# Performance work log

Measured on AMD Instinct MI355X. Metric: run time of the kernel, lower is better.

## Reference

```python
import jax, jax.numpy as jnp
import numpy as np
from jax import lax

POOL_OUT = 20  # SOCA AdaptiveAvgPool2d((20,20))
MID = 16       # out_channel // 2
BN_EPS = 1e-3


def _pool_matrix(n, out):
    # Row-stochastic matrix replicating torch AdaptiveAvgPool2d bin boundaries:
    # start = floor(i*n/out), end = ceil((i+1)*n/out)
    P = np.zeros((out, n), np.float32)
    for i in range(out):
        s = (i * n) // out
        e = -((-(i + 1) * n) // out)
        P[i, s:e] = 1.0 / (e - s)
    return jnp.asarray(P)


def setup_inputs() -> dict:
    key = jax.random.key(0)
    ks = jax.random.split(key, 5)
    B, C, H, W = 16, 256, 128, 128
    OC = 32
    x = jax.random.normal(ks[0], (B, C, H, W), dtype=jnp.float32)
    linear_w = jax.random.normal(ks[1], (C, C), dtype=jnp.float32) * (1.0 / np.sqrt(C))
    linear_b = jnp.zeros((C,), jnp.float32)
    lsa_w = jax.random.normal(ks[2], (1, 2, 7, 7), dtype=jnp.float32) * 0.1  # Conv2d(2,1,7) no bias
    conv_w = jax.random.normal(ks[3], (OC, OC, 3, 3), dtype=jnp.float32) * (1.0 / np.sqrt(OC * 9))
    conv_b = jnp.zeros((OC,), jnp.float32)
    bn_gamma = jnp.ones((OC,), jnp.float32)
    bn_beta = jnp.zeros((OC,), jnp.float32)
    return {"x": x, "linear_w": linear_w, "linear_b": linear_b, "lsa_w": lsa_w,
            "conv_w": conv_w, "conv_b": conv_b, "bn_gamma": bn_gamma, "bn_beta": bn_beta}


def _bsa_forward(x, linear_w, linear_b, lsa_w, conv_w, conv_b, bn_gamma, bn_beta):
    b, c, h, w = x.shape
    # ---- SOCA: second-order channel attention ----
    PH = _pool_matrix(h, POOL_OUT)
    PW = _pool_matrix(w, POOL_OUT)
    xp = jnp.einsum('oh,bchw,pw->bcop', PH, x, PW)          # (b,c,20,20)
    n = POOL_OUT * POOL_OUT
    v = xp.reshape(b, c, n).transpose(0, 2, 1)               # (b,400,c)
    vc = v - v.mean(axis=1, keepdims=True)
    cov = jnp.einsum('bnc,bnd->bcd', vc, vc) / (n - 1)       # (b,c,c)
    feat = cov.mean(axis=2)                                  # (b,c)
    attn = jax.nn.sigmoid(feat @ linear_w.T + linear_b)      # (b,c)
    # ---- channel scoring / top-k selection ----
    score = attn.mean(axis=0)                                # (c,)
    score_id = jnp.argsort(-score)                           # descending
    max_id = jnp.sort(score_id[:MID])                        # (MID,)
    x1 = jnp.take(x, max_id, axis=1) * (1.0 + score[max_id])[None, :, None, None]
    # ---- grouped channel mean (c divisible by MID by construction) ----
    g = c // MID
    x2 = x.reshape(b, MID, g, h, w).mean(axis=2)             # (b,MID,h,w)
    xc = jnp.concatenate([x1, x2], axis=1)                   # (b,32,h,w)
    # ---- LSA spatial attention ----
    s = jnp.concatenate([xc.mean(axis=1, keepdims=True),
                         xc.max(axis=1, keepdims=True)], axis=1)  # (b,2,h,w)
    a = lax.conv_general_dilated(s, lsa_w, (1, 1), [(3, 3), (3, 3)],
                                 dimension_numbers=('NCHW', 'OIHW', 'NCHW'))
    xa = xc * jax.nn.sigmoid(a)
    # ---- CBA: conv(3x3, stride 2) + BN(train stats) + SiLU ----
    y = lax.conv_general_dilated(xa, conv_w, (2, 2), [(1, 1), (1, 1)],
                                 dimension_numbers=('NCHW', 'OIHW', 'NCHW'))
    y = y + conv_b[None, :, None, None]
    mu = y.mean(axis=(0, 2, 3))
    var = y.var(axis=(0, 2, 3))
    yn = (y - mu[None, :, None, None]) * lax.rsqrt(var + BN_EPS)[None, :, None, None]
    yn = yn * bn_gamma[None, :, None, None] + bn_beta[None, :, None, None]
    return yn * jax.nn.sigmoid(yn)  # SiLU


def reference(x, linear_w, linear_b, lsa_w, conv_w, conv_b, bn_gamma, bn_beta):
    return _bsa_forward(x, linear_w, linear_b, lsa_w, conv_w, conv_b, bn_gamma, bn_beta)
```

## Files before the change

### kernel.cpp

```cpp
#include <hip/hip_runtime.h>
#include <math.h>

#define B_ 16
#define C_ 256
#define H_ 128
#define W_ 128
#define HW_ (H_*W_)
#define PO 20
#define NPOOL (PO*PO)
#define MID_ 16
#define OC_ 32
#define OH_ 64
#define OW_ 64
#define BN_EPS 1e-3f

#define OFF_XP     0
#define OFF_SN     1638400
#define OFF_SCORE  1648896
#define OFF_BNSUM  1649184
#define OFF_BNSQ   1649216
#define OFF_SMEAN  1649248
#define OFF_SMAX   1911392
#define OFF_SIGA   2173536
#define OFF_XC     2435680

__device__ __forceinline__ int bin_s(int p) { return (p * 128) / 20; }
__device__ __forceinline__ int bin_e(int p) { return ((p + 1) * 128 + 19) / 20; }

__global__ __launch_bounds__(256) void k_pool2(const float* __restrict__ x,
                                               float* __restrict__ xp,
                                               float* __restrict__ sn,
                                               float* __restrict__ xc) {
  __shared__ float tmp[2][64 * 21];
  const int blk = blockIdx.x;
  const int b = blk >> 5, g = (blk >> 1) & 15, rh = blk & 1;
  const int tid = threadIdx.x;
  const int hl = tid >> 2, q = tid & 3;
  const int hg = rh * 64 + hl;
  const float* rowbase = x + (size_t)(b * C_) * HW_ + (size_t)hg * W_ + q * 32;

  float4 xacc[8];
#pragma unroll
  for (int j = 0; j < 8; ++j) xacc[j] = make_float4(0.f, 0.f, 0.f, 0.f);
  float snacc = 0.f;

  float4 cur[8], nxt[8];
  {
    const float4* s4 = (const float4*)(rowbase + (size_t)(g * 16) * HW_);
#pragma unroll
    for (int j = 0; j < 8; ++j) cur[j] = s4[j];
  }

#pragma unroll
  for (int k = 0; k < 16; ++k) {
    if (k < 15) {
      const float4* s4 = (const float4*)(rowbase + (size_t)(g * 16 + k + 1) * HW_);
#pragma unroll
      for (int j = 0; j < 8; ++j) nxt[j] = s4[j];
    }
    const int c = g * 16 + k;
    float bin[5];
#pragma unroll
    for (int p = 0; p < 5; ++p) bin[p] = 0.f;
#pragma unroll
    for (int j = 0; j < 8; ++j) {
      float4 v = cur[j];
      xacc[j].x += v.x; xacc[j].y += v.y; xacc[j].z += v.z; xacc[j].w += v.w;
      const float c4[4] = {v.x, v.y, v.z, v.w};
#pragma unroll
      for (int kk = 0; kk < 4; ++kk) {
        const int cc = 4 * j + kk;
#pragma unroll
        for (int p = 0; p < 5; ++p) {
          const int S = (p * 32) / 5;
          const int E = ((p + 1) * 32 + 4) / 5;
          if (cc >= S && cc < E) bin[p] += c4[kk];
        }
      }
    }
    float* tb = tmp[k & 1];
#pragma unroll
    for (int p = 0; p < 5; ++p) {
      const int S = (p * 32) / 5, E = ((p + 1) * 32 + 4) / 5;
      tb[hl * 21 + q * 5 + p] = bin[p] / (float)(E - S);
    }
    asm volatile("s_waitcnt lgkmcnt(0)\n\ts_barrier" ::: "memory");
    if (tid < 200) {
      const int ol = tid / 20, p = tid % 20;
      const int o = rh * 10 + ol;
      const int rs_ = bin_s(o), re_ = bin_e(o);
      float s = 0.f;
      for (int r = rs_; r < re_; ++r) s += tb[(r - rh * 64) * 21 + p];
      float v = s / (float)(re_ - rs_);
      xp[(size_t)(b * C_ + c) * NPOOL + o * PO + p] = v;
      snacc += v;
    }
    if (k < 15) {
#pragma unroll
      for (int j = 0; j < 8; ++j) cur[j] = nxt[j];
    }
  }
  if (tid < 200) atomicAdd(&sn[b * NPOOL + rh * 200 + tid], snacc);
  float4* dst = (float4*)(xc + (size_t)(b * OC_ + MID_ + g) * HW_ + (size_t)hg * W_ + q * 32);
#pragma unroll
  for (int j = 0; j < 8; ++j) {
    float4 v = xacc[j];
    v.x *= 0.0625f; v.y *= 0.0625f; v.z *= 0.0625f; v.w *= 0.0625f;
    dst[j] = v;
  }
}

__global__ __launch_bounds__(256) void k_featattn(const float* __restrict__ xp,
                                                  const float* __restrict__ sn,
                                                  const float* __restrict__ lw,
                                                  const float* __restrict__ lb,
                                                  float* __restrict__ score) {
  const int b = blockIdx.x;
  const int tid = threadIdx.x;
  __shared__ float snl[NPOOL];
  __shared__ float red[256];
  __shared__ float featl[C_];
  for (int i = tid; i < NPOOL; i += 256) snl[i] = sn[b * NPOOL + i];
  __syncthreads();
  const float4* row4 = (const float4*)(xp + (size_t)(b * C_ + tid) * NPOOL);
  float rs = 0.f, dot = 0.f;
#pragma unroll 4
  for (int n = 0; n < NPOOL / 4; ++n) {
    float4 v = row4[n];
    rs += v.x + v.y + v.z + v.w;
    dot += v.x * snl[4 * n] + v.y * snl[4 * n + 1]
         + v.z * snl[4 * n + 2] + v.w * snl[4 * n + 3];
  }
  red[tid] = rs;
  __syncthreads();
  for (int s = 128; s > 0; s >>= 1) {
    if (tid < s) red[tid] += red[tid + s];
    __syncthreads();
  }
  const float totm = red[0] / (float)NPOOL;
  featl[tid] = (dot - totm * rs) / ((float)(NPOOL - 1) * (float)C_);
  __syncthreads();
  const float4* wrow = (const float4*)(lw + (size_t)tid * C_);
  float z = 0.f;
#pragma unroll 4
  for (int i = 0; i < C_ / 4; ++i) {
    float4 w = wrow[i];
    z += w.x * featl[4 * i] + w.y * featl[4 * i + 1]
       + w.z * featl[4 * i + 2] + w.w * featl[4 * i + 3];
  }
  z += lb[tid];
  float sig = 1.0f / (1.0f + expf(-z));
  atomicAdd(&score[tid], sig * (1.0f / (float)B_));
}

__global__ __launch_bounds__(256) void k_build(const float* __restrict__ x,
                                               const float* __restrict__ score,
                                               float* __restrict__ xc,
                                               float* __restrict__ smean,
                                               float* __restrict__ smax) {
  __shared__ float ss[C_];
  __shared__ int flag[C_];
  __shared__ int mid_s[MID_];
  __shared__ float sc_s[MID_];
  __shared__ float4 ps[128], pm[128];
  const int tid = threadIdx.x;
  ss[tid] = score[tid];
  __syncthreads();
  {
    float my = ss[tid];
    int rank = 0;
    for (int k = 0; k < C_; ++k) {
      float v = ss[k];
      rank += (v > my || (v == my && k < tid)) ? 1 : 0;
    }
    flag[tid] = (rank < MID_) ? 1 : 0;
    __syncthreads();
    if (rank < MID_) {
      int pos = 0;
      for (int k = 0; k < tid; ++k) pos += flag[k];
      mid_s[pos] = tid;
      sc_s[pos] = 1.0f + my;
    }
  }
  __syncthreads();
  const int p = tid & 127, s = tid >> 7;
  const int P = blockIdx.x * 128 + p;
  const int b = P >> 12, pix4 = P & 4095;
  const float4* xb = (const float4*)x + (size_t)(b * C_) * (HW_ / 4) + pix4;
  float4* xcb = (float4*)xc + (size_t)(b * OC_) * (HW_ / 4) + pix4;
  float4 ms = make_float4(0.f, 0.f, 0.f, 0.f);
  float4 mx = make_float4(-INFINITY, -INFINITY, -INFINITY, -INFINITY);
#pragma unroll
  for (int mi = 0; mi < 8; ++mi) {
    int m = s * 8 + mi;
    float4 t = xb[(size_t)mid_s[m] * (HW_ / 4)];
    float sc = sc_s[m];
    t.x *= sc; t.y *= sc; t.z *= sc; t.w *= sc;
    xcb[(size_t)m * (HW_ / 4)] = t;
    ms.x += t.x; ms.y += t.y; ms.z += t.z; ms.w += t.w;
    mx.x = fmaxf(mx.x, t.x); mx.y = fmaxf(mx.y, t.y);
    mx.z = fmaxf(mx.z, t.z); mx.w = fmaxf(mx.w, t.w);
  }
#pragma unroll
  for (int gi = 0; gi < 8; ++gi) {
    float4 t = xcb[(size_t)(MID_ + s * 8 + gi) * (HW_ / 4)];
    ms.x += t.x; ms.y += t.y; ms.z += t.z; ms.w += t.w;
    mx.x = fmaxf(mx.x, t.x); mx.y = fmaxf(mx.y, t.y);
    mx.z = fmaxf(mx.z, t.z); mx.w = fmaxf(mx.w, t.w);
  }
  if (s == 1) { ps[p] = ms; pm[p] = mx; }
  __syncthreads();
  if (s == 0) {
    float4 a = ps[p], m2 = pm[p];
    ms.x = (ms.x + a.x) * (1.f / 32.f); ms.y = (ms.y + a.y) * (1.f / 32.f);
    ms.z = (ms.z + a.z) * (1.f / 32.f); ms.w = (ms.w + a.w) * (1.f / 32.f);
    mx.x = fmaxf(mx.x, m2.x); mx.y = fmaxf(mx.y, m2.y);
    mx.z = fmaxf(mx.z, m2.z); mx.w = fmaxf(mx.w, m2.w);
    ((float4*)smean)[P] = ms;
    ((float4*)smax)[P] = mx;
  }
}

__global__ __launch_bounds__(256) void k_lsa(const float* __restrict__ smean,
                                             const float* __restrict__ smax,
                                             const float* __restrict__ lsa_w,
                                             float* __restrict__ siga) {
  __shared__ float w0[49], w1[49];
  if (threadIdx.x < 49) {
    w0[threadIdx.x] = lsa_w[threadIdx.x];
    w1[threadIdx.x] = lsa_w[49 + threadIdx.x];
  }
  __syncthreads();
  int idx = blockIdx.x * 256 + threadIdx.x;
  int b = idx >> 14;
  int pix = idx & (HW_ - 1);
  int h = pix >> 7, w = pix & 127;
  const float* pm = smean + (size_t)b * HW_;
  const float* px = smax + (size_t)b * HW_;
  float acc = 0.f;
  for (int kh = 0; kh < 7; ++kh) {
    int ih = h + kh - 3;
    if (ih < 0 || ih >= H_) continue;
    for (int kw = 0; kw < 7; ++kw) {
      int iw = w + kw - 3;
      if (iw < 0 || iw >= W_) continue;
      int p = ih * W_ + iw;
      acc += pm[p] * w0[kh * 7 + kw] + px[p] * w1[kh * 7 + kw];
    }
  }
  siga[idx] = 1.0f / (1.0f + __expf(-acc));
}

__global__ __launch_bounds__(256) void k_conv(const float* __restrict__ xc,
                                              const float* __restrict__ siga,
                                              const float* __restrict__ conv_w,
                                              const float* __restrict__ conv_b,
                                              float* __restrict__ out,
                                              float* __restrict__ bnsum,
                                              float* __restrict__ bnsq) {
  __shared__ __attribute__((aligned(16))) float in_lds[4 * 5 * 132];
  __shared__ float sg_lds[5 * 132];
  __shared__ float w_lds[288 * 33];
  const int tid = threadIdx.x;
  const int oc = tid & 31;
  const int g = tid >> 5;
  const int b = blockIdx.x >> 5;
  const int oh0 = (blockIdx.x & 31) * 2;
  const int ih0 = 2 * oh0 - 1;

  for (int i = tid; i < 288 * 32; i += 256) {
    int oc_ = i / 288, rem = i % 288;
    w_lds[rem * 33 + oc_] = conv_w[i];
  }
  const float* sgb = siga + (size_t)b * HW_;
  for (int i = tid; i < 5 * 132; i += 256) {
    int r = i / 132, col = i % 132;
    int ih = ih0 + r, iw = col - 1;
    float v = 0.f;
    if (ih >= 0 && ih < H_ && iw >= 0 && iw < W_) v = sgb[ih * W_ + iw];
    sg_lds[i] = v;
  }

  float acc[2][8];
#pragma unroll
  for (int a = 0; a < 2; ++a)
#pragma unroll
    for (int o = 0; o < 8; ++o) acc[a][o] = 0.f;

  for (int chunk = 0; chunk < 8; ++chunk) {
    __syncthreads();
    for (int i = tid; i < 4 * 5 * 132; i += 256) {
      int icl = i / 660;
      int rem = i % 660;
      int r = rem / 132, col = rem % 132;
      int ih = ih0 + r, iw = col - 1;
      float v = 0.f;
      if (ih >= 0 && ih < H_ && iw >= 0 && iw < W_) {
        v = xc[((size_t)(b * OC_) + (chunk * 4 + icl)) * HW_ + ih * W_ + iw] * sg_lds[rem];
      }
      in_lds[i] = v;
    }
    __syncthreads();
#pragma unroll
    for (int icl = 0; icl < 4; ++icl) {
      float wr[9];
      const int wb = (chunk * 4 + icl) * 9 * 33 + oc;
#pragma unroll
      for (int t = 0; t < 9; ++t) wr[t] = w_lds[wb + t * 33];
#pragma unroll
      for (int r = 0; r < 5; ++r) {
        float f[20] __attribute__((aligned(16)));
        const float4* s4 = (const float4*)&in_lds[(icl * 5 + r) * 132 + 16 * g];
#pragma unroll
        for (int j = 0; j < 5; ++j) ((float4*)f)[j] = s4[j];
#pragma unroll
        for (int ohl = 0; ohl < 2; ++ohl) {
          const int kh = r - 2 * ohl;
          if (kh < 0 || kh > 2) continue;
          float w0 = wr[kh * 3 + 0];
          float w1 = wr[kh * 3 + 1];
          float w2 = wr[kh * 3 + 2];
#pragma unroll
          for (int o = 0; o < 8; ++o)
            acc[ohl][o] += f[2 * o] * w0 + f[2 * o + 1] * w1 + f[2 * o + 2] * w2;
        }
      }
    }
  }

  float bias = conv_b[oc];
  float lsum = 0.f, lsq = 0.f;
  float* outp = out + ((size_t)(b * OC_) + oc) * (OH_ * OW_) + (size_t)oh0 * OW_ + g * 8;
#pragma unroll
  for (int ohl = 0; ohl < 2; ++ohl) {
    float vout[8] __attribute__((aligned(16)));
#pragma unroll
    for (int o = 0; o < 8; ++o) {
      float v = acc[ohl][o] + bias;
      vout[o] = v;
      lsum += v;
      lsq += v * v;
    }
    *((float4*)(outp + ohl * OW_)) = *(float4*)&vout[0];
    *((float4*)(outp + ohl * OW_ + 4)) = *(float4*)&vout[4];
  }
  __syncthreads();
  in_lds[tid] = lsum;
  in_lds[256 + tid] = lsq;
  __syncthreads();
  if (tid < 32) {
    float t = 0.f, tq = 0.f;
#pragma unroll
    for (int gg = 0; gg < 8; ++gg) {
      t += in_lds[gg * 32 + tid];
      tq += in_lds[256 + gg * 32 + tid];
    }
    atomicAdd(&bnsum[tid], t);
    atomicAdd(&bnsq[tid], tq);
  }
}

__global__ __launch_bounds__(256) void k_apply(float* __restrict__ out,
                                               const float* __restrict__ sum,
                                               const float* __restrict__ sq,
                                               const float* __restrict__ gamma,
                                               const float* __restrict__ beta) {
  __shared__ float ssc[OC_], ssh[OC_];
  if (threadIdx.x < OC_) {
    int i = threadIdx.x;
    const float N = (float)(B_ * OH_ * OW_);
    float mu = sum[i] / N;
    float var = sq[i] / N - mu * mu;
    float sc = gamma[i] / sqrtf(var + BN_EPS);
    ssc[i] = sc;
    ssh[i] = beta[i] - mu * sc;
  }
  __syncthreads();
  int idx4 = blockIdx.x * 256 + threadIdx.x;
  int oc = (idx4 >> 10) & 31;
  float sc = ssc[oc], sh = ssh[oc];
  float4 v = ((float4*)out)[idx4];
  float t;
  t = v.x * sc + sh; v.x = t / (1.0f + __expf(-t));
  t = v.y * sc + sh; v.y = t / (1.0f + __expf(-t));
  t = v.z * sc + sh; v.z = t / (1.0f + __expf(-t));
  t = v.w * sc + sh; v.w = t / (1.0f + __expf(-t));
  ((float4*)out)[idx4] = v;
}

extern "C" void kernel_launch(void* const* d_in, const int* in_sizes, int n_in,
                              void* d_out, int out_size, void* d_ws, size_t ws_size,
                              hipStream_t stream) {
  const float* x      = (const float*)d_in[0];
  const float* lw     = (const float*)d_in[1];
  const float* lb     = (const float*)d_in[2];
  const float* lsa_w  = (const float*)d_in[3];
  const float* conv_w = (const float*)d_in[4];
  const float* conv_b = (const float*)d_in[5];
  const float* gamma  = (const float*)d_in[6];
  const float* beta   = (const float*)d_in[7];
  float* out = (float*)d_out;
  float* ws = (float*)d_ws;

  hipMemsetAsync(ws + OFF_SN, 0,
                 (size_t)(OFF_BNSQ + OC_ - OFF_SN) * sizeof(float), stream);

  k_pool2<<<512, 256, 0, stream>>>(x, ws + OFF_XP, ws + OFF_SN, ws + OFF_XC);
  k_featattn<<<B_, 256, 0, stream>>>(ws + OFF_XP, ws + OFF_SN, lw, lb, ws + OFF_SCORE);
  k_build<<<512, 256, 0, stream>>>(x, ws + OFF_SCORE, ws + OFF_XC,
                                   ws + OFF_SMEAN, ws + OFF_SMAX);
  k_lsa<<<1024, 256, 0, stream>>>(ws + OFF_SMEAN, ws + OFF_SMAX, lsa_w, ws + OFF_SIGA);
  k_conv<<<512, 256, 0, stream>>>(ws + OFF_XC, ws + OFF_SIGA, conv_w, conv_b, out,
                                  ws + OFF_BNSUM, ws + OFF_BNSQ);
  k_apply<<<2048, 256, 0, stream>>>(out, ws + OFF_BNSUM, ws + OFF_BNSQ, gamma, beta);
}
```

Before: 504.2 us.

## Fuse all stages into one persistent kernel with software grid barriers

Replaces the six separate kernel launches with a single 512-block kernel. The stages are separated by atomic-counter grid barriers in workspace memory. The feature/attention step is also spread over all 512 blocks instead of 16, using warp-level reductions and an extra per-batch totm atomic. The goal is to remove launch gaps and the serialised low-parallelism featattn kernel. In exchange it drops the register double-buffering prefetch in the pool stage and relies on all 512 blocks being co-resident for the spin barriers to work. The barrier has a guard timeout that could silently break ordering.

New measurement: 898.8 us. +78.3%, slower.

```diff
diff --git a/kernel.cpp b/kernel.cpp
--- a/kernel.cpp
+++ b/kernel.cpp
@@ -16,376 +16,407 @@
 
 #define OFF_XP     0
 #define OFF_SN     1638400
+#define OFF_BAR    1644800
 #define OFF_SCORE  1648896
+#define OFF_TOTM   1649152
 #define OFF_BNSUM  1649184
 #define OFF_BNSQ   1649216
 #define OFF_SMEAN  1649248
 #define OFF_SMAX   1911392
 #define OFF_SIGA   2173536
 #define OFF_XC     2435680
+#define OFF_RS     10824288
+#define OFF_DOT    10828384
 
 __device__ __forceinline__ int bin_s(int p) { return (p * 128) / 20; }
 __device__ __forceinline__ int bin_e(int p) { return ((p + 1) * 128 + 19) / 20; }
 
-__global__ __launch_bounds__(256) void k_pool2(const float* __restrict__ x,
-                                               float* __restrict__ xp,
-                                               float* __restrict__ sn,
-                                               float* __restrict__ xc) {
-  __shared__ float tmp[2][64 * 21];
+__device__ __forceinline__ void gbar(unsigned* bar, unsigned target) {
+  __syncthreads();
+  if (threadIdx.x == 0) {
+    __threadfence();
+    __hip_atomic_fetch_add(bar, 1u, __ATOMIC_RELEASE, __HIP_MEMORY_SCOPE_AGENT);
+    long guard = 0;
+    while (__hip_atomic_load(bar, __ATOMIC_ACQUIRE, __HIP_MEMORY_SCOPE_AGENT) < target) {
+      __builtin_amdgcn_s_sleep(8);
+      if (++guard > (1L << 22)) break;
+    }
+  }
+  __syncthreads();
+}
+
+__global__ __launch_bounds__(256, 2) void mega(
+    const float* __restrict__ x, const float* __restrict__ lw,
+    const float* __restrict__ lb, const float* __restrict__ lsa_w,
+    const float* __restrict__ conv_w, const float* __restrict__ conv_b,
+    const float* __restrict__ gamma, const float* __restrict__ beta,
+    float* __restrict__ out, float* __restrict__ ws) {
+  __shared__ __attribute__((aligned(16))) float smem[13000];
   const int blk = blockIdx.x;
-  const int b = blk >> 5, g = (blk >> 1) & 15, rh = blk & 1;
   const int tid = threadIdx.x;
-  const int hl = tid >> 2, q = tid & 3;
-  const int hg = rh * 64 + hl;
-  const float* rowbase = x + (size_t)(b * C_) * HW_ + (size_t)hg * W_ + q * 32;
-
-  float4 xacc[8];
-#pragma unroll
-  for (int j = 0; j < 8; ++j) xacc[j] = make_float4(0.f, 0.f, 0.f, 0.f);
-  float snacc = 0.f;
-
-  float4 cur[8], nxt[8];
-  {
-    const float4* s4 = (const float4*)(rowbase + (size_t)(g * 16) * HW_);
-#pragma unroll
-    for (int j = 0; j < 8; ++j) cur[j] = s4[j];
-  }
-
-#pragma unroll
-  for (int k = 0; k < 16; ++k) {
-    if (k < 15) {
-      const float4* s4 = (const float4*)(rowbase + (size_t)(g * 16 + k + 1) * HW_);
-#pragma unroll
-      for (int j = 0; j < 8; ++j) nxt[j] = s4[j];
-    }
-    const int c = g * 16 + k;
-    float bin[5];
-#pragma unroll
-    for (int p = 0; p < 5; ++p) bin[p] = 0.f;
+  float* xp    = ws + OFF_XP;
+  float* sn    = ws + OFF_SN;
+  unsigned* bar = (unsigned*)(ws + OFF_BAR);
+  float* score = ws + OFF_SCORE;
+  float* totm  = ws + OFF_TOTM;
+  float* bnsum = ws + OFF_BNSUM;
+  float* bnsq  = ws + OFF_BNSQ;
+  float* smean = ws + OFF_SMEAN;
+  float* smax  = ws + OFF_SMAX;
+  float* siga  = ws + OFF_SIGA;
+  float* xc    = ws + OFF_XC;
+  float* rsb   = ws + OFF_RS;
+  float* dotb  = ws + OFF_DOT;
+
+  {
+    float (*tmp)[64 * 21] = (float (*)[64 * 21])smem;
+    const int b = blk >> 5, g = (blk >> 1) & 15, rh = blk & 1;
+    const int hl = tid >> 2, q = tid & 3;
+    const int hg = rh * 64 + hl;
+    const float* rowbase = x + (size_t)(b * C_) * HW_ + (size_t)hg * W_ + q * 32;
+
+    float4 xacc[8];
+#pragma unroll
+    for (int j = 0; j < 8; ++j) xacc[j] = make_float4(0.f, 0.f, 0.f, 0.f);
+    float snacc = 0.f;
+
+    for (int k = 0; k < 16; ++k) {
+      const int c = g * 16 + k;
+      const float4* src4 = (const float4*)(rowbase + (size_t)c * HW_);
+      float bin[5];
+#pragma unroll
+      for (int p = 0; p < 5; ++p) bin[p] = 0.f;
+#pragma unroll
+      for (int j = 0; j < 8; ++j) {
+        float4 v = src4[j];
+        xacc[j].x += v.x; xacc[j].y += v.y; xacc[j].z += v.z; xacc[j].w += v.w;
+        const float c4[4] = {v.x, v.y, v.z, v.w};
+#pragma unroll
+        for (int kk = 0; kk < 4; ++kk) {
+          const int cc = 4 * j + kk;
+#pragma unroll
+          for (int p = 0; p < 5; ++p) {
+            const int S = (p * 32) / 5;
+            const int E = ((p + 1) * 32 + 4) / 5;
+            if (cc >= S && cc < E) bin[p] += c4[kk];
+          }
+        }
+      }
+      float* tb = tmp[k & 1];
+#pragma unroll
+      for (int p = 0; p < 5; ++p) {
+        const int S = (p * 32) / 5, E = ((p + 1) * 32 + 4) / 5;
+        tb[hl * 21 + q * 5 + p] = bin[p] / (float)(E - S);
+      }
+      __syncthreads();
+      if (tid < 200) {
+        const int ol = tid / 20, p = tid % 20;
+        const int o = rh * 10 + ol;
+        const int rs_ = bin_s(o), re_ = bin_e(o);
+        float s = 0.f;
+        for (int r = rs_; r < re_; ++r) s += tb[(r - rh * 64) * 21 + p];
+        float v = s / (float)(re_ - rs_);
+        xp[(size_t)(b * C_ + c) * NPOOL + o * PO + p] = v;
+        snacc += v;
+      }
+    }
+    if (tid < 200) atomicAdd(&sn[b * NPOOL + rh * 200 + tid], snacc);
+    float4* dst = (float4*)(xc + (size_t)(b * OC_ + MID_ + g) * HW_ + (size_t)hg * W_ + q * 32);
 #pragma unroll
     for (int j = 0; j < 8; ++j) {
-      float4 v = cur[j];
-      xacc[j].x += v.x; xacc[j].y += v.y; xacc[j].z += v.z; xacc[j].w += v.w;
-      const float c4[4] = {v.x, v.y, v.z, v.w};
-#pragma unroll
-      for (int kk = 0; kk < 4; ++kk) {
-        const int cc = 4 * j + kk;
-#pragma unroll
-        for (int p = 0; p < 5; ++p) {
-          const int S = (p * 32) / 5;
-          const int E = ((p + 1) * 32 + 4) / 5;
-          if (cc >= S && cc < E) bin[p] += c4[kk];
+      float4 v = xacc[j];
+      v.x *= 0.0625f; v.y *= 0.0625f; v.z *= 0.0625f; v.w *= 0.0625f;
+      dst[j] = v;
+    }
+  }
+  gbar(bar, 512);
+
+  {
+    float* snl  = smem;
+    float* part = smem + 400;
+    const int bb = blk >> 5, sub = blk & 31;
+    const int cl = tid >> 5, lane = tid & 31;
+    const int c = sub * 8 + cl;
+    for (int i = tid; i < NPOOL; i += 256) snl[i] = sn[bb * NPOOL + i];
+    __syncthreads();
+    const float* row = xp + (size_t)(bb * C_ + c) * NPOOL;
+    float rs = 0.f, dt = 0.f;
+    for (int n = lane; n < NPOOL; n += 32) {
+      float v = row[n];
+      rs += v;
+      dt += v * snl[n];
+    }
+#pragma unroll
+    for (int o = 16; o > 0; o >>= 1) {
+      rs += __shfl_down(rs, o, 32);
+      dt += __shfl_down(dt, o, 32);
+    }
+    if (lane == 0) {
+      rsb[bb * C_ + c] = rs;
+      dotb[bb * C_ + c] = dt;
+      part[cl] = rs;
+    }
+    __syncthreads();
+    if (tid == 0) {
+      float s = 0.f;
+#pragma unroll
+      for (int i = 0; i < 8; ++i) s += part[i];
+      atomicAdd(&totm[bb], s);
+    }
+  }
+  gbar(bar, 1024);
+
+  {
+    float* rs_l  = smem;
+    float* dot_l = smem + 256;
+    const int bb = blk >> 5, sub = blk & 31;
+    rs_l[tid]  = rsb[bb * C_ + tid];
+    dot_l[tid] = dotb[bb * C_ + tid];
+    __syncthreads();
+    const float t = totm[bb] * (1.0f / (float)NPOOL);
+    const int j = sub * 8 + (tid >> 5), lane = tid & 31;
+    const float* wrow = lw + (size_t)j * C_;
+    const float INV = 1.0f / ((float)(NPOOL - 1) * (float)C_);
+    float z = 0.f;
+#pragma unroll
+    for (int i0 = 0; i0 < 8; ++i0) {
+      int i = lane + 32 * i0;
+      z += wrow[i] * ((dot_l[i] - t * rs_l[i]) * INV);
+    }
+#pragma unroll
+    for (int o = 16; o > 0; o >>= 1) z += __shfl_down(z, o, 32);
+    if (lane == 0) {
+      float zf = z + lb[j];
+      float sig = 1.0f / (1.0f + expf(-zf));
+      atomicAdd(&score[j], sig * (1.0f / (float)B_));
+    }
+  }
+  gbar(bar, 1536);
+
+  {
+    float* ss    = smem;
+    int* flag    = (int*)(smem + 256);
+    int* mid_s   = (int*)(smem + 512);
+    float* sc_s  = smem + 528;
+    float4* ps   = (float4*)(smem + 544);
+    float4* pm   = (float4*)(smem + 1056);
+    ss[tid] = score[tid];
+    __syncthreads();
+    {
+      float my = ss[tid];
+      int rank = 0;
+      for (int k = 0; k < C_; ++k) {
+        float v = ss[k];
+        rank += (v > my || (v == my && k < tid)) ? 1 : 0;
+      }
+      flag[tid] = (rank < MID_) ? 1 : 0;
+      __syncthreads();
+      if (rank < MID_) {
+        int pos = 0;
+        for (int k = 0; k < tid; ++k) pos += flag[k];
+        mid_s[pos] = tid;
+        sc_s[pos] = 1.0f + my;
+      }
+    }
+    __syncthreads();
+    const int p = tid & 127, s = tid >> 7;
+    const int P = blk * 128 + p;
+    const int b = P >> 12, pix4 = P & 4095;
+    const float4* xb = (const float4*)x + (size_t)(b * C_) * (HW_ / 4) + pix4;
+    float4* xcb = (float4*)xc + (size_t)(b * OC_) * (HW_ / 4) + pix4;
+    float4 ms = make_float4(0.f, 0.f, 0.f, 0.f);
+    float4 mx = make_float4(-INFINITY, -INFINITY, -INFINITY, -INFINITY);
+#pragma unroll
+    for (int mi = 0; mi < 8; ++mi) {
+      int m = s * 8 + mi;
+      float4 t = xb[(size_t)mid_s[m] * (HW_ / 4)];
+      float sc = sc_s[m];
+      t.x *= sc; t.y *= sc; t.z *= sc; t.w *= sc;
+      xcb[(size_t)m * (HW_ / 4)] = t;
+      ms.x += t.x; ms.y += t.y; ms.z += t.z; ms.w += t.w;
+      mx.x = fmaxf(mx.x, t.x); mx.y = fmaxf(mx.y, t.y);
+      mx.z = fmaxf(mx.z, t.z); mx.w = fmaxf(mx.w, t.w);
+    }
+#pragma unroll
+    for (int gi = 0; gi < 8; ++gi) {
+      float4 t = xcb[(size_t)(MID_ + s * 8 + gi) * (HW_ / 4)];
+      ms.x += t.x; ms.y += t.y; ms.z += t.z; ms.w += t.w;
+      mx.x = fmaxf(mx.x, t.x); mx.y = fmaxf(mx.y, t.y);
+      mx.z = fmaxf(mx.z, t.z); mx.w = fmaxf(mx.w, t.w);
+    }
+    if (s == 1) { ps[p] = ms; pm[p] = mx; }
+    __syncthreads();
+    if (s == 0) {
+      float4 a = ps[p], m2 = pm[p];
+      ms.x = (ms.x + a.x) * (1.f / 32.f); ms.y = (ms.y + a.y) * (1.f / 32.f);
+      ms.z = (ms.z + a.z) * (1.f / 32.f); ms.w = (ms.w + a.w) * (1.f / 32.f);
+      mx.x = fmaxf(mx.x, m2.x); mx.y = fmaxf(mx.y, m2.y);
+      mx.z = fmaxf(mx.z, m2.z); mx.w = fmaxf(mx.w, m2.w);
+      ((float4*)smean)[P] = ms;
+      ((float4*)smax)[P] = mx;
+    }
+  }
+  gbar(bar, 2048);
+
+  {
+    float* w0 = smem;
+    float* w1 = smem + 49;
+    if (tid < 49) { w0[tid] = lsa_w[tid]; w1[tid] = lsa_w[49 + tid]; }
+    __syncthreads();
+#pragma unroll
+    for (int u = 0; u < 2; ++u) {
+      int idx = (blk * 2 + u) * 256 + tid;
+      int b = idx >> 14;
+      int pix = idx & (HW_ - 1);
+      int h = pix >> 7, w = pix & 127;
+      const float* pmn = smean + (size_t)b * HW_;
+      const float* pxm = smax + (size_t)b * HW_;
+      float acc = 0.f;
+      for (int kh = 0; kh < 7; ++kh) {
+        int ih = h + kh - 3;
+        if (ih < 0 || ih >= H_) continue;
+        for (int kw = 0; kw < 7; ++kw) {
+          int iw = w + kw - 3;
+          if (iw < 0 || iw >= W_) continue;
+          int p = ih * W_ + iw;
+          acc += pmn[p] * w0[kh * 7 + kw] + pxm[p] * w1[kh * 7 + kw];
         }
       }
-    }
-    float* tb = tmp[k & 1];
-#pragma unroll
-    for (int p = 0; p < 5; ++p) {
-      const int S = (p * 32) / 5, E = ((p + 1) * 32 + 4) / 5;
-      tb[hl * 21 + q * 5 + p] = bin[p] / (float)(E - S);
-    }
-    asm volatile("s_waitcnt lgkmcnt(0)\n\ts_barrier" ::: "memory");
-    if (tid < 200) {
-      const int ol = tid / 20, p = tid % 20;
-      const int o = rh * 10 + ol;
-      const int rs_ = bin_s(o), re_ = bin_e(o);
-      float s = 0.f;
-      for (int r = rs_; r < re_; ++r) s += tb[(r - rh * 64) * 21 + p];
-      float v = s / (float)(re_ - rs_);
-      xp[(size_t)(b * C_ + c) * NPOOL + o * PO + p] = v;
-      snacc += v;
-    }
-    if (k < 15) {
-#pragma unroll
-      for (int j = 0; j < 8; ++j) cur[j] = nxt[j];
-    }
-  }
-  if (tid < 200) atomicAdd(&sn[b * NPOOL + rh * 200 + tid], snacc);
-  float4* dst = (float4*)(xc + (size_t)(b * OC_ + MID_ + g) * HW_ + (size_t)hg * W_ + q * 32);
-#pragma unroll
-  for (int j = 0; j < 8; ++j) {
-    float4 v = xacc[j];
-    v.x *= 0.0625f; v.y *= 0.0625f; v.z *= 0.0625f; v.w *= 0.0625f;
-    dst[j] = v;
-  }
-}
-
-__global__ __launch_bounds__(256) void k_featattn(const float* __restrict__ xp,
-                                                  const float* __restrict__ sn,
-                                                  const float* __restrict__ lw,
-                                                  const float* __restrict__ lb,
-                                                  float* __restrict__ score) {
-  const int b = blockIdx.x;
-  const int tid = threadIdx.x;
-  __shared__ float snl[NPOOL];
-  __shared__ float red[256];
-  __shared__ float featl[C_];
-  for (int i = tid; i < NPOOL; i += 256) snl[i] = sn[b * NPOOL + i];
-  __syncthreads();
-  const float4* row4 = (const float4*)(xp + (size_t)(b * C_ + tid) * NPOOL);
-  float rs = 0.f, dot = 0.f;
-#pragma unroll 4
-  for (int n = 0; n < NPOOL / 4; ++n) {
-    float4 v = row4[n];
-    rs += v.x + v.y + v.z + v.w;
-    dot += v.x * snl[4 * n] + v.y * snl[4 * n + 1]
-         + v.z * snl[4 * n + 2] + v.w * snl[4 * n + 3];
-  }
-  red[tid] = rs;
-  __syncthreads();
-  for (int s = 128; s > 0; s >>= 1) {
-    if (tid < s) red[tid] += red[tid + s];
-    __syncthreads();
-  }
-  const float totm = red[0] / (float)NPOOL;
-  featl[tid] = (dot - totm * rs) / ((float)(NPOOL - 1) * (float)C_);
-  __syncthreads();
-  const float4* wrow = (const float4*)(lw + (size_t)tid * C_);
-  float z = 0.f;
-#pragma unroll 4
-  for (int i = 0; i < C_ / 4; ++i) {
-    float4 w = wrow[i];
-    z += w.x * featl[4 * i] + w.y * featl[4 * i + 1]
-       + w.z * featl[4 * i + 2] + w.w * featl[4 * i + 3];
-  }
-  z += lb[tid];
-  float sig = 1.0f / (1.0f + expf(-z));
-  atomicAdd(&score[tid], sig * (1.0f / (float)B_));
-}
-
-__global__ __launch_bounds__(256) void k_build(const float* __restrict__ x,
-                                               const float* __restrict__ score,
-                                               float* __restrict__ xc,
-                                               float* __restrict__ smean,
-                                               float* __restrict__ smax) {
-  __shared__ float ss[C_];
-  __shared__ int flag[C_];
-  __shared__ int mid_s[MID_];
-  __shared__ float sc_s[MID_];
-  __shared__ float4 ps[128], pm[128];
-  const int tid = threadIdx.x;
-  ss[tid] = score[tid];
-  __syncthreads();
-  {
-    float my = ss[tid];
-    int rank = 0;
-    for (int k = 0; k < C_; ++k) {
-      float v = ss[k];
-      rank += (v > my || (v == my && k < tid)) ? 1 : 0;
-    }
-    flag[tid] = (rank < MID_) ? 1 : 0;
-    __syncthreads();
-    if (rank < MID_) {
-      int pos = 0;
-      for (int k = 0; k < tid; ++k) pos += flag[k];
-      mid_s[pos] = tid;
-      sc_s[pos] = 1.0f + my;
-    }
-  }
-  __syncthreads();
-  const int p = tid & 127, s = tid >> 7;
-  const int P = blockIdx.x * 128 + p;
-  const int b = P >> 12, pix4 = P & 4095;
-  const float4* xb = (const float4*)x + (size_t)(b * C_) * (HW_ / 4) + pix4;
-  float4* xcb = (float4*)xc + (size_t)(b * OC_) * (HW_ / 4) + pix4;
-  float4 ms = make_float4(0.f, 0.f, 0.f, 0.f);
-  float4 mx = make_float4(-INFINITY, -INFINITY, -INFINITY, -INFINITY);
-#pragma unroll
-  for (int mi = 0; mi < 8; ++mi) {
-    int m = s * 8 + mi;
-    float4 t = xb[(size_t)mid_s[m] * (HW_ / 4)];
-    float sc = sc_s[m];
-    t.x *= sc; t.y *= sc; t.z *= sc; t.w *= sc;
-    xcb[(size_t)m * (HW_ / 4)] = t;
-    ms.x += t.x; ms.y += t.y; ms.z += t.z; ms.w += t.w;
-    mx.x = fmaxf(mx.x, t.x); mx.y = fmaxf(mx.y, t.y);
-    mx.z = fmaxf(mx.z, t.z); mx.w = fmaxf(mx.w, t.w);
-  }
-#pragma unroll
-  for (int gi = 0; gi < 8; ++gi) {
-    float4 t = xcb[(size_t)(MID_ + s * 8 + gi) * (HW_ / 4)];
-    ms.x += t.x; ms.y += t.y; ms.z += t.z; ms.w += t.w;
-    mx.x = fmaxf(mx.x, t.x); mx.y = fmaxf(mx.y, t.y);
-    mx.z = fmaxf(mx.z, t.z); mx.w = fmaxf(mx.w, t.w);
-  }
-  if (s == 1) { ps[p] = ms; pm[p] = mx; }
-  __syncthreads();
-  if (s == 0) {
-    float4 a = ps[p], m2 = pm[p];
-    ms.x = (ms.x + a.x) * (1.f / 32.f); ms.y = (ms.y + a.y) * (1.f / 32.f);
-    ms.z = (ms.z + a.z) * (1.f / 32.f); ms.w = (ms.w + a.w) * (1.f / 32.f);
-    mx.x = fmaxf(mx.x, m2.x); mx.y = fmaxf(mx.y, m2.y);
-    mx.z = fmaxf(mx.z, m2.z); mx.w = fmaxf(mx.w, m2.w);
-    ((float4*)smean)[P] = ms;
-    ((float4*)smax)[P] = mx;
-  }
-}
-
-__global__ __launch_bounds__(256) void k_lsa(const float* __restrict__ smean,
-                                             const float* __restrict__ smax,
-                                             const float* __restrict__ lsa_w,
-                                             float* __restrict__ siga) {
-  __shared__ float w0[49], w1[49];
-  if (threadIdx.x < 49) {
-    w0[threadIdx.x] = lsa_w[threadIdx.x];
-    w1[threadIdx.x] = lsa_w[49 + threadIdx.x];
-  }
-  __syncthreads();
-  int idx = blockIdx.x * 256 + threadIdx.x;
-  int b = idx >> 14;
-  int pix = idx & (HW_ - 1);
-  int h = pix >> 7, w = pix & 127;
-  const float* pm = smean + (size_t)b * HW_;
-  const float* px = smax + (size_t)b * HW_;
-  float acc = 0.f;
-  for (int kh = 0; kh < 7; ++kh) {
-    int ih = h + kh - 3;
-    if (ih < 0 || ih >= H_) continue;
-    for (int kw = 0; kw < 7; ++kw) {
-      int iw = w + kw - 3;
-      if (iw < 0 || iw >= W_) continue;
-      int p = ih * W_ + iw;
-      acc += pm[p] * w0[kh * 7 + kw] + px[p] * w1[kh * 7 + kw];
-    }
-  }
-  siga[idx] = 1.0f / (1.0f + __expf(-acc));
-}
-
-__global__ __launch_bounds__(256) void k_conv(const float* __restrict__ xc,
-                                              const float* __restrict__ siga,
-                                              const float* __restrict__ conv_w,
-                                              const float* __restrict__ conv_b,
-                                              float* __restrict__ out,
-                                              float* __restrict__ bnsum,
-                                              float* __restrict__ bnsq) {
-  __shared__ __attribute__((aligned(16))) float in_lds[4 * 5 * 132];
-  __shared__ float sg_lds[5 * 132];
-  __shared__ float w_lds[288 * 33];
-  const int tid = threadIdx.x;
-  const int oc = tid & 31;
-  const int g = tid >> 5;
-  const int b = blockIdx.x >> 5;
-  const int oh0 = (blockIdx.x & 31) * 2;
-  const int ih0 = 2 * oh0 - 1;
-
-  for (int i = tid; i < 288 * 32; i += 256) {
-    int oc_ = i / 288, rem = i % 288;
-    w_lds[rem * 33 + oc_] = conv_w[i];
-  }
-  const float* sgb = siga + (size_t)b * HW_;
-  for (int i = tid; i < 5 * 132; i += 256) {
-    int r = i / 132, col = i % 132;
-    int ih = ih0 + r, iw = col - 1;
-    float v = 0.f;
-    if (ih >= 0 && ih < H_ && iw >= 0 && iw < W_) v = sgb[ih * W_ + iw];
-    sg_lds[i] = v;
-  }
-
-  float acc[2][8];
-#pragma unroll
-  for (int a = 0; a < 2; ++a)
-#pragma unroll
-    for (int o = 0; o < 8; ++o) acc[a][o] = 0.f;
-
-  for (int chunk = 0; chunk < 8; ++chunk) {
-    __syncthreads();
-    for (int i = tid; i < 4 * 5 * 132; i += 256) {
-      int icl = i / 660;
-      int rem = i % 660;
-      int r = rem / 132, col = rem % 132;
+      siga[idx] = 1.0f / (1.0f + __expf(-acc));
+    }
+    __syncthreads();
+  }
+  gbar(bar, 2560);
+
+  {
+    float* in_lds = smem;
+    float* sg_lds = smem + 2640;
+    float* w_lds  = smem + 3300;
+    const int oc = tid & 31;
+    const int g = tid >> 5;
+    const int b = blk >> 5;
+    const int oh0 = (blk & 31) * 2;
+    const int ih0 = 2 * oh0 - 1;
+
+    for (int i = tid; i < 288 * 32; i += 256) {
+      int oc_ = i / 288, rem = i % 288;
+      w_lds[rem * 33 + oc_] = conv_w[i];
+    }
+    const float* sgb = siga + (size_t)b * HW_;
+    for (int i = tid; i < 5 * 132; i += 256) {
+      int r = i / 132, col = i % 132;
       int ih = ih0 + r, iw = col - 1;
       float v = 0.f;
-      if (ih >= 0 && ih < H_ && iw >= 0 && iw < W_) {
-        v = xc[((size_t)(b * OC_) + (chunk * 4 + icl)) * HW_ + ih * W_ + iw] * sg_lds[rem];
-      }
-      in_lds[i] = v;
-    }
-    __syncthreads();
-#pragma unroll
-    for (int icl = 0; icl < 4; ++icl) {
-      float wr[9];
-      const int wb = (chunk * 4 + icl) * 9 * 33 + oc;
-#pragma unroll
-      for (int t = 0; t < 9; ++t) wr[t] = w_lds[wb + t * 33];
-#pragma unroll
-      for (int r = 0; r < 5; ++r) {
-        float f[20] __attribute__((aligned(16)));
-        const float4* s4 = (const float4*)&in_lds[(icl * 5 + r) * 132 + 16 * g];
-#pragma unroll
-        for (int j = 0; j < 5; ++j) ((float4*)f)[j] = s4[j];
-#pragma unroll
-        for (int ohl = 0; ohl < 2; ++ohl) {
-          const int kh = r - 2 * ohl;
-          if (kh < 0 || kh > 2) continue;
-          float w0 = wr[kh * 3 + 0];
-          float w1 = wr[kh * 3 + 1];
-          float w2 = wr[kh * 3 + 2];
-#pragma unroll
-          for (int o = 0; o < 8; ++o)
-            acc[ohl][o] += f[2 * o] * w0 + f[2 * o + 1] * w1 + f[2 * o + 2] * w2;
+      if (ih >= 0 && ih < H_ && iw >= 0 && iw < W_) v = sgb[ih * W_ + iw];
+      sg_lds[i] = v;
+    }
+
+    float acc[2][8];
+#pragma unroll
+    for (int a = 0; a < 2; ++a)
+#pragma unroll
+      for (int o = 0; o < 8; ++o) acc[a][o] = 0.f;
+
+    for (int chunk = 0; chunk < 8; ++chunk) {
+      __syncthreads();
+      for (int i = tid; i < 4 * 5 * 132; i += 256) {
+        int icl = i / 660;
+        int rem = i % 660;
+        int r = rem / 132, col = rem % 132;
+        int ih = ih0 + r, iw = col - 1;
+        float v = 0.f;
+        if (ih >= 0 && ih < H_ && iw >= 0 && iw < W_) {
+          v = xc[((size_t)(b * OC_) + (chunk * 4 + icl)) * HW_ + ih * W_ + iw] * sg_lds[rem];
         }
-      }
-    }
-  }
-
-  float bias = conv_b[oc];
-  float lsum = 0.f, lsq = 0.f;
-  float* outp = out + ((size_t)(b * OC_) + oc) * (OH_ * OW_) + (size_t)oh0 * OW_ + g * 8;
-#pragma unroll
-  for (int ohl = 0; ohl < 2; ++ohl) {
-    float vout[8] __attribute__((aligned(16)));
-#pragma unroll
-    for (int o = 0; o < 8; ++o) {
-      float v = acc[ohl][o] + bias;
-      vout[o] = v;
-      lsum += v;
-      lsq += v * v;
-    }
-    *((float4*)(outp + ohl * OW_)) = *(float4*)&vout[0];
-    *((float4*)(outp + ohl * OW_ + 4)) = *(float4*)&vout[4];
-  }
-  __syncthreads();
-  in_lds[tid] = lsum;
-  in_lds[256 + tid] = lsq;
-  __syncthreads();
-  if (tid < 32) {
-    float t = 0.f, tq = 0.f;
-#pragma unroll
-    for (int gg = 0; gg < 8; ++gg) {
-      t += in_lds[gg * 32 + tid];
-      tq += in_lds[256 + gg * 32 + tid];
-    }
-    atomicAdd(&bnsum[tid], t);
-    atomicAdd(&bnsq[tid], tq);
-  }
-}
-
-__global__ __launch_bounds__(256) void k_apply(float* __restrict__ out,
-                                               const float* __restrict__ sum,
-                                               const float* __restrict__ sq,
-                                               const float* __restrict__ gamma,
-                                               const float* __restrict__ beta) {
-  __shared__ float ssc[OC_], ssh[OC_];
-  if (threadIdx.x < OC_) {
-    int i = threadIdx.x;
-    const float N = (float)(B_ * OH_ * OW_);
-    float mu = sum[i] / N;
-    float var = sq[i] / N - mu * mu;
-    float sc = gamma[i] / sqrtf(var + BN_EPS);
-    ssc[i] = sc;
-    ssh[i] = beta[i] - mu * sc;
-  }
-  __syncthreads();
-  int idx4 = blockIdx.x * 256 + threadIdx.x;
-  int oc = (idx4 >> 10) & 31;
-  float sc = ssc[oc], sh = ssh[oc];
-  float4 v = ((float4*)out)[idx4];
-  float t;
-  t = v.x * sc + sh; v.x = t / (1.0f + __expf(-t));
-  t = v.y * sc + sh; v.y = t / (1.0f + __expf(-t));
-  t = v.z * sc + sh; v.z = t / (1.0f + __expf(-t));
-  t = v.w * sc + sh; v.w = t / (1.0f + __expf(-t));
-  ((float4*)out)[idx4] = v;
+        in_lds[i] = v;
+      }
+      __syncthreads();
+#pragma unroll
+      for (int icl = 0; icl < 4; ++icl) {
+        float wr[9];
+        const int wb = (chunk * 4 + icl) * 9 * 33 + oc;
+#pragma unroll
+        for (int t = 0; t < 9; ++t) wr[t] = w_lds[wb + t * 33];
+#pragma unroll
+        for (int r = 0; r < 5; ++r) {
+          float f[20] __attribute__((aligned(16)));
+          const float4* s4 = (const float4*)&in_lds[(icl * 5 + r) * 132 + 16 * g];
+#pragma unroll
+          for (int j = 0; j < 5; ++j) ((float4*)f)[j] = s4[j];
+#pragma unroll
+          for (int ohl = 0; ohl < 2; ++ohl) {
+            const int kh = r - 2 * ohl;
+            if (kh < 0 || kh > 2) continue;
+            float w0 = wr[kh * 3 + 0];
+            float w1 = wr[kh * 3 + 1];
+            float w2 = wr[kh * 3 + 2];
+#pragma unroll
+            for (int o = 0; o < 8; ++o)
+              acc[ohl][o] += f[2 * o] * w0 + f[2 * o + 1] * w1 + f[2 * o + 2] * w2;
+          }
+        }
+      }
+    }
+
+    float bias = conv_b[oc];
+    float lsum = 0.f, lsq = 0.f;
+    float* outp = out + ((size_t)(b * OC_) + oc) * (OH_ * OW_) + (size_t)oh0 * OW_ + g * 8;
+#pragma unroll
+    for (int ohl = 0; ohl < 2; ++ohl) {
+      float vout[8] __attribute__((aligned(16)));
+#pragma unroll
+      for (int o = 0; o < 8; ++o) {
+        float v = acc[ohl][o] + bias;
+        vout[o] = v;
+        lsum += v;
+        lsq += v * v;
+      }
+      *((float4*)(outp + ohl * OW_)) = *(float4*)&vout[0];
+      *((float4*)(outp + ohl * OW_ + 4)) = *(float4*)&vout[4];
+    }
+    __syncthreads();
+    in_lds[tid] = lsum;
+    in_lds[256 + tid] = lsq;
+    __syncthreads();
+    if (tid < 32) {
+      float t = 0.f, tq = 0.f;
+#pragma unroll
+      for (int gg = 0; gg < 8; ++gg) {
+        t += in_lds[gg * 32 + tid];
+        tq += in_lds[256 + gg * 32 + tid];
+      }
+      atomicAdd(&bnsum[tid], t);
+      atomicAdd(&bnsq[tid], tq);
+    }
+  }
+  gbar(bar, 3072);
+
+  {
+    float* ssc = smem;
+    float* ssh = smem + 32;
+    if (tid < OC_) {
+      const float N = (float)(B_ * OH_ * OW_);
+      float mu = bnsum[tid] / N;
+      float var = bnsq[tid] / N - mu * mu;
+      float sc = gamma[tid] / sqrtf(var + BN_EPS);
+      ssc[tid] = sc;
+      ssh[tid] = beta[tid] - mu * sc;
+    }
+    __syncthreads();
+#pragma unroll
+    for (int u = 0; u < 4; ++u) {
+      int idx4 = (blk * 4 + u) * 256 + tid;
+      int oc = (idx4 >> 10) & 31;
+      float sc = ssc[oc], sh = ssh[oc];
+      float4 v = ((float4*)out)[idx4];
+      float t;
+      t = v.x * sc + sh; v.x = t / (1.0f + __expf(-t));
+      t = v.y * sc + sh; v.y = t / (1.0f + __expf(-t));
+      t = v.z * sc + sh; v.z = t / (1.0f + __expf(-t));
+      t = v.w * sc + sh; v.w = t / (1.0f + __expf(-t));
+      ((float4*)out)[idx4] = v;
+    }
+  }
 }
 
 extern "C" void kernel_launch(void* const* d_in, const int* in_sizes, int n_in,
@@ -405,12 +436,6 @@
   hipMemsetAsync(ws + OFF_SN, 0,
                  (size_t)(OFF_BNSQ + OC_ - OFF_SN) * sizeof(float), stream);
 
-  k_pool2<<<512, 256, 0, stream>>>(x, ws + OFF_XP, ws + OFF_SN, ws + OFF_XC);
-  k_featattn<<<B_, 256, 0, stream>>>(ws + OFF_XP, ws + OFF_SN, lw, lb, ws + OFF_SCORE);
-  k_build<<<512, 256, 0, stream>>>(x, ws + OFF_SCORE, ws + OFF_XC,
-                                   ws + OFF_SMEAN, ws + OFF_SMAX);
-  k_lsa<<<1024, 256, 0, stream>>>(ws + OFF_SMEAN, ws + OFF_SMAX, lsa_w, ws + OFF_SIGA);
-  k_conv<<<512, 256, 0, stream>>>(ws + OFF_XC, ws + OFF_SIGA, conv_w, conv_b, out,
-                                  ws + OFF_BNSUM, ws + OFF_BNSQ);
-  k_apply<<<2048, 256, 0, stream>>>(out, ws + OFF_BNSUM, ws + OFF_BNSQ, gamma, beta);
+  mega<<<512, 256, 0, stream>>>(x, lw, lb, lsa_w, conv_w, conv_b,
+                                gamma, beta, out, ws);
 }
```
